# Performance work log

Measured on AMD Instinct MI355X. Metric: run time of the kernel, lower is better.

## Reference

```python
import jax, jax.numpy as jnp
import numpy as np

N, E, D, ED, L, B = 100000, 1600000, 128, 16, 5, 64
EPS = 1e-5


def _layer_norm(x, w, b):
    mu = jnp.mean(x, axis=-1, keepdims=True)
    var = jnp.mean((x - mu) ** 2, axis=-1, keepdims=True)
    return (x - mu) * jax.lax.rsqrt(var + EPS) * w + b


def setup_inputs() -> dict:
    key = jax.random.key(0)
    ks = jax.random.split(key, 10)
    sc = 0.05
    s = jax.random.normal(ks[0], (N, D), jnp.float32)
    edge_index = jax.random.randint(ks[1], (2, E), 0, N, dtype=jnp.int64)
    edge_attr = jax.random.normal(ks[2], (E, ED), jnp.float32)
    batch = jnp.sort(jax.random.randint(ks[3], (N,), 0, B, dtype=jnp.int64))
    return dict(
        s=s, edge_index=edge_index, edge_attr=edge_attr, batch=batch,
        ln_w=jnp.ones((L, D), jnp.float32),
        ln_b=jnp.zeros((L, D), jnp.float32),
        eW1=jax.random.normal(ks[4], (L, 2 * D + ED, ED), jnp.float32) * sc,
        eb1=jnp.zeros((L, ED), jnp.float32),
        eW2=jax.random.normal(ks[5], (L, ED, ED), jnp.float32) * sc,
        eb2=jnp.zeros((L, ED), jnp.float32),
        nW1=jax.random.normal(ks[6], (L, D + ED, D), jnp.float32) * sc,
        nb1=jnp.zeros((L, D), jnp.float32),
        nW2=jax.random.normal(ks[7], (L, D, D), jnp.float32) * sc,
        nb2=jnp.zeros((L, D), jnp.float32),
    )


def reference(s, edge_index, edge_attr, batch, ln_w, ln_b, eW1, eb1, eW2, eb2, nW1, nb1, nW2, nb2):
    src, dst = edge_index[0], edge_index[1]
    n = s.shape[0]
    num_layers = ln_w.shape[0]
    # scatter-mean denominator (in-degree, clamped to 1)
    deg = jax.ops.segment_sum(jnp.ones((edge_index.shape[1],), s.dtype), dst, num_segments=n)
    deg = jnp.maximum(deg, 1.0)[:, None]
    for i in range(num_layers):
        # per-node LayerNorm over feature dim (vector channel is None)
        s = _layer_norm(s, ln_w[i], ln_b[i])
        # edge message: gather endpoints, concat with edge_attr -> [E, 2D+ED]
        m = jnp.concatenate([s[src], s[dst], edge_attr], axis=-1)
        edge_attr = jax.nn.silu(m @ eW1[i] + eb1[i]) @ eW2[i] + eb2[i]
        # scatter-mean aggregate to destination nodes -> [N, ED]
        agg = jax.ops.segment_sum(edge_attr, dst, num_segments=n) / deg
        h = jnp.concatenate([s, agg], axis=-1)
        out = jax.nn.silu(h @ nW1[i] + nb1[i]) @ nW2[i] + nb2[i]  # discarded, as in original
    return s, edge_attr
```

## Files before the change

kernel.cpp:

```cpp
#include <hip/hip_runtime.h>

#define N_NODES 100000
#define N_EDGES 1600000
#define DIM     128
#define EDIM    16
#define NLAYERS 5

typedef unsigned short ushort_t;
typedef short bf16x8 __attribute__((ext_vector_type(8)));
typedef float f32x4  __attribute__((ext_vector_type(4)));

__device__ __forceinline__ ushort_t f2bf(float f) {
    union { float f; unsigned int i; } c; c.f = f;
    unsigned int r = c.i + 0x7fffu + ((c.i >> 16) & 1u);
    return (ushort_t)(r >> 16);
}
__device__ __forceinline__ float lo_bf(unsigned int w) {
    union { unsigned int i; float f; } c; c.i = w << 16; return c.f;
}
__device__ __forceinline__ float hi_bf(unsigned int w) {
    union { unsigned int i; float f; } c; c.i = w & 0xffff0000u; return c.f;
}
__device__ __forceinline__ unsigned int pk_bf16(float lo, float hi) {
    unsigned int r;
    asm("v_cvt_pk_bf16_f32 %0, %1, %2" : "=v"(r) : "v"(lo), "v"(hi));
    return r;
}
__device__ __forceinline__ bf16x8 pk8(f32x4 a, f32x4 b) {
    union { unsigned int w[4]; bf16x8 v; } c;
    c.w[0] = pk_bf16(a[0], a[1]); c.w[1] = pk_bf16(a[2], a[3]);
    c.w[2] = pk_bf16(b[0], b[1]); c.w[3] = pk_bf16(b[2], b[3]);
    return c.v;
}
__device__ __forceinline__ float fast_silu(float x) {
    return x * __builtin_amdgcn_rcpf(1.0f + __expf(-x));
}
__device__ __forceinline__ void lds_fence() {
    asm volatile("s_waitcnt lgkmcnt(0)" ::: "memory");
    __builtin_amdgcn_sched_barrier(0);
}

__global__ void swizzle_weights(const float* __restrict__ eW1,
                                const float* __restrict__ eW2,
                                const float* __restrict__ eb1,
                                const float* __restrict__ eb2,
                                ushort_t* __restrict__ w1s,
                                ushort_t* __restrict__ w2s,
                                ushort_t* __restrict__ wcs,
                                float* __restrict__ bcs) {
    int id = blockIdx.x * 256 + threadIdx.x;
    const int base = NLAYERS * 10 * 64;
    if (id < base) {
        int lane = id & 63;
        int t10 = id >> 6;
        int layer = t10 / 10, t = t10 % 10;
        int n = lane & 15, quad = lane >> 4;
        if (t < 9) {
            ushort_t* dst = w1s + ((size_t)(layer * 9 + t) * 64 + lane) * 8;
            #pragma unroll
            for (int j = 0; j < 8; ++j) {
                int k = t * 32 + quad * 8 + j;
                dst[j] = (k < 2 * DIM + EDIM)
                           ? f2bf(eW1[((size_t)layer * 272 + k) * 16 + n])
                           : (ushort_t)0;
            }
        } else {
            ushort_t* dst = w2s + ((size_t)layer * 64 + lane) * 8;
            #pragma unroll
            for (int j = 0; j < 8; ++j) {
                int k = quad * 8 + j;
                dst[j] = (k < EDIM) ? f2bf(eW2[((size_t)layer * 16 + k) * 16 + n])
                                    : (ushort_t)0;
            }
        }
    } else if (id < base + 4 * 64) {
        int id2 = id - base;
        int l = id2 >> 6;
        int lane = id2 & 63, n = lane & 15, quad = lane >> 4;
        ushort_t* dst = wcs + ((size_t)l * 64 + lane) * 8;
        #pragma unroll
        for (int j = 0; j < 8; ++j) {
            int r = quad * 8 + j;
            float acc = 0.f;
            if (r < EDIM)
                for (int k = 0; k < EDIM; ++k)
                    acc += eW2[((size_t)l * 16 + r) * 16 + k]
                         * eW1[((size_t)(l + 1) * 272 + 256 + k) * 16 + n];
            dst[j] = (r < EDIM) ? f2bf(acc) : (ushort_t)0;
        }
    } else if (id < base + 4 * 64 + 64) {
        int id2 = id - base - 4 * 64;
        int l = id2 >> 4, n = id2 & 15;
        float acc = eb1[(l + 1) * 16 + n];
        for (int k = 0; k < EDIM; ++k)
            acc += eb2[l * 16 + k] * eW1[((size_t)(l + 1) * 272 + 256 + k) * 16 + n];
        bcs[l * 16 + n] = acc;
    }
}

__global__ __launch_bounds__(256) void ln_uv(
        const float* __restrict__ sin, float* __restrict__ sout,
        const float* __restrict__ lnw, const float* __restrict__ lnb,
        const ushort_t* __restrict__ w1s,
        ushort_t* __restrict__ u_buf, ushort_t* __restrict__ v_buf,
        int l0, int l1, int lstr) {
    const int wv = threadIdx.x >> 6, lane = threadIdx.x & 63;
    const int m = lane & 15, quad = lane >> 4;
    const int tile = blockIdx.x * 4 + wv;
    if (tile >= N_NODES / 16) return;
    const int node = tile * 16 + m;

    float x[32];
    {
        const float* row = sin + (size_t)node * DIM + quad * 8;
        #pragma unroll
        for (int t = 0; t < 4; ++t) {
            f32x4 a = *(const f32x4*)(row + t * 32);
            f32x4 b = *(const f32x4*)(row + t * 32 + 4);
            #pragma unroll
            for (int j = 0; j < 4; ++j) { x[t * 8 + j] = a[j]; x[t * 8 + 4 + j] = b[j]; }
        }
    }

    for (int li = l0; li < l1; ++li) {
        float s = 0.f;
        #pragma unroll
        for (int k = 0; k < 32; ++k) s += x[k];
        s += __shfl_xor(s, 16); s += __shfl_xor(s, 32);
        float mu = s * (1.0f / DIM);
        float ss = 0.f;
        #pragma unroll
        for (int k = 0; k < 32; ++k) { float d = x[k] - mu; ss += d * d; }
        ss += __shfl_xor(ss, 16); ss += __shfl_xor(ss, 32);
        float rs = rsqrtf(ss * (1.0f / DIM) + 1e-5f);

        const float* w = lnw + (size_t)li * DIM + quad * 8;
        const float* b = lnb + (size_t)li * DIM + quad * 8;
        f32x4 au = {0.f, 0.f, 0.f, 0.f}, av = {0.f, 0.f, 0.f, 0.f};
        #pragma unroll
        for (int t = 0; t < 4; ++t) {
            f32x4 wa = *(const f32x4*)(w + t * 32), wb = *(const f32x4*)(w + t * 32 + 4);
            f32x4 ba = *(const f32x4*)(b + t * 32), bb = *(const f32x4*)(b + t * 32 + 4);
            #pragma unroll
            for (int j = 0; j < 4; ++j) {
                x[t * 8 + j]     = (x[t * 8 + j]     - mu) * rs * wa[j] + ba[j];
                x[t * 8 + 4 + j] = (x[t * 8 + 4 + j] - mu) * rs * wb[j] + bb[j];
            }
            f32x4 ya, yb;
            #pragma unroll
            for (int j = 0; j < 4; ++j) { ya[j] = x[t * 8 + j]; yb[j] = x[t * 8 + 4 + j]; }
            bf16x8 af = pk8(ya, yb);
            bf16x8 bu = *(const bf16x8*)(w1s + ((size_t)(li * 9 + t)     * 64 + lane) * 8);
            bf16x8 bv = *(const bf16x8*)(w1s + ((size_t)(li * 9 + 4 + t) * 64 + lane) * 8);
            au = __builtin_amdgcn_mfma_f32_16x16x32_bf16(bu, af, au, 0, 0, 0);
            av = __builtin_amdgcn_mfma_f32_16x16x32_bf16(bv, af, av, 0, 0, 0);
        }
        size_t rec = ((size_t)node * lstr + (li - l0)) * EDIM + quad * 4;
        uint2 tu; tu.x = pk_bf16(au[0], au[1]); tu.y = pk_bf16(au[2], au[3]);
        uint2 tv; tv.x = pk_bf16(av[0], av[1]); tv.y = pk_bf16(av[2], av[3]);
        *(uint2*)(u_buf + rec) = tu;
        *(uint2*)(v_buf + rec) = tv;
    }

    float* orow = sout + (size_t)node * DIM + quad * 8;
    #pragma unroll
    for (int t = 0; t < 4; ++t) {
        f32x4 a, b;
        #pragma unroll
        for (int j = 0; j < 4; ++j) { a[j] = x[t * 8 + j]; b[j] = x[t * 8 + 4 + j]; }
        *(f32x4*)(orow + t * 32) = a;
        *(f32x4*)(orow + t * 32 + 4) = b;
    }
}

template<int NL>
__global__ __launch_bounds__(256) void edge_fused(
        const float* __restrict__ ea_in, float* __restrict__ ea_out,
        const int* __restrict__ ei,
        const ushort_t* __restrict__ u_buf, const ushort_t* __restrict__ v_buf,
        const ushort_t* __restrict__ w1s, const ushort_t* __restrict__ w2s,
        const ushort_t* __restrict__ wcs, const float* __restrict__ bcs,
        const float* __restrict__ eb1, const float* __restrict__ eb2,
        int l0) {
    __shared__ ushort_t tbH[4][16 * 24];
    const int wv = threadIdx.x >> 6, lane = threadIdx.x & 63;
    const int m = lane & 15, quad = lane >> 4;

    const bf16x8 w1f0 = *(const bf16x8*)(w1s + (((size_t)l0 * 9 + 8) * 64 + lane) * 8);
    const bf16x8 w2f  = *(const bf16x8*)(w2s + ((size_t)(l0 + NL - 1) * 64 + lane) * 8);
    bf16x8 wcf[NL > 1 ? NL - 1 : 1];
    #pragma unroll
    for (int l = 1; l < NL; ++l)
        wcf[l - 1] = *(const bf16x8*)(wcs + ((size_t)(l0 + l - 1) * 64 + lane) * 8);
    f32x4 bx[NL], b2v;
    #pragma unroll
    for (int r = 0; r < 4; ++r) {
        bx[0][r] = eb1[l0 * EDIM + quad * 4 + r];
        b2v[r]   = eb2[(l0 + NL - 1) * EDIM + quad * 4 + r];
    }
    #pragma unroll
    for (int l = 1; l < NL; ++l)
        #pragma unroll
        for (int r = 0; r < 4; ++r)
            bx[l][r] = bcs[(l0 + l - 1) * EDIM + quad * 4 + r];

    ushort_t* tlH = tbH[wv];
    const bf16x8 zf = {0, 0, 0, 0, 0, 0, 0, 0};
    const f32x4 z4 = {0.f, 0.f, 0.f, 0.f};
    const int nTiles = N_EDGES / 64;
    const int stride = gridDim.x;

    int tile = blockIdx.x;
    if (tile >= nTiles) return;

    uint2 gu[NL], gv[NL];
    f32x4 ea_a = z4, ea_b = z4;
    int es_n, ed_n;
    {
        const int e0 = tile * 64 + wv * 16 + m;
        const int es = ei[e0];
        const int ed = ei[N_EDGES + e0];
        #pragma unroll
        for (int l = 0; l < NL; ++l) {
            gu[l] = *(const uint2*)(u_buf + ((size_t)es * NL + l) * EDIM + quad * 4);
            gv[l] = *(const uint2*)(v_buf + ((size_t)ed * NL + l) * EDIM + quad * 4);
        }
        if (quad < 2) {
            const float* ep = ea_in + (size_t)e0 * EDIM + quad * 8;
            ea_a = *(const f32x4*)ep; ea_b = *(const f32x4*)(ep + 4);
        }
        const int t1 = tile + stride;
        const int e1 = (t1 < nTiles ? t1 : tile) * 64 + wv * 16 + m;
        es_n = ei[e1];
        ed_n = ei[N_EDGES + e1];
    }

    for (; tile < nTiles; tile += stride) {
        const int tn = tile + stride;
        const bool hn = tn < nTiles;
        const int tc = hn ? tn : tile;

        uint2 gun[NL], gvn[NL];
        #pragma unroll
        for (int l = 0; l < NL; ++l) {
            gun[l] = *(const uint2*)(u_buf + ((size_t)es_n * NL + l) * EDIM + quad * 4);
            gvn[l] = *(const uint2*)(v_buf + ((size_t)ed_n * NL + l) * EDIM + quad * 4);
        }
        f32x4 ean_a = z4, ean_b = z4;
        {
            const int en = tc * 64 + wv * 16 + m;
            if (quad < 2) {
                const float* ep = ea_in + (size_t)en * EDIM + quad * 8;
                ean_a = *(const f32x4*)ep; ean_b = *(const f32x4*)(ep + 4);
            }
        }
        int es_nn, ed_nn;
        {
            const int t2 = tn + stride;
            const int e2 = (t2 < nTiles ? t2 : tc) * 64 + wv * 16 + m;
            es_nn = ei[e2];
            ed_nn = ei[N_EDGES + e2];
        }

        f32x4 hv;
        {
            bf16x8 af = zf;
            if (quad < 2) af = pk8(ea_a, ea_b);
            f32x4 acc = __builtin_amdgcn_mfma_f32_16x16x32_bf16(w1f0, af, z4, 0, 0, 0);
            hv[0] = fast_silu(acc[0] + lo_bf(gu[0].x) + lo_bf(gv[0].x) + bx[0][0]);
            hv[1] = fast_silu(acc[1] + hi_bf(gu[0].x) + hi_bf(gv[0].x) + bx[0][1]);
            hv[2] = fast_silu(acc[2] + lo_bf(gu[0].y) + lo_bf(gv[0].y) + bx[0][2]);
            hv[3] = fast_silu(acc[3] + hi_bf(gu[0].y) + hi_bf(gv[0].y) + bx[0][3]);
        }
        #pragma unroll
        for (int l = 1; l < NL; ++l) {
            uint2 hw; hw.x = pk_bf16(hv[0], hv[1]); hw.y = pk_bf16(hv[2], hv[3]);
            *(uint2*)(tlH + m * 24 + quad * 4) = hw;
            lds_fence();
            bf16x8 hf = zf;
            if (quad < 2) hf = *(const bf16x8*)(tlH + m * 24 + quad * 8);

            f32x4 acc = __builtin_amdgcn_mfma_f32_16x16x32_bf16(wcf[l - 1], hf, z4, 0, 0, 0);
            hv[0] = fast_silu(acc[0] + lo_bf(gu[l].x) + lo_bf(gv[l].x) + bx[l][0]);
            hv[1] = fast_silu(acc[1] + hi_bf(gu[l].x) + hi_bf(gv[l].x) + bx[l][1]);
            hv[2] = fast_silu(acc[2] + lo_bf(gu[l].y) + lo_bf(gv[l].y) + bx[l][2]);
            hv[3] = fast_silu(acc[3] + hi_bf(gu[l].y) + hi_bf(gv[l].y) + bx[l][3]);
        }
        f32x4 y;
        {
            uint2 hw; hw.x = pk_bf16(hv[0], hv[1]); hw.y = pk_bf16(hv[2], hv[3]);
            *(uint2*)(tlH + m * 24 + quad * 4) = hw;
            lds_fence();
            bf16x8 hf = zf;
            if (quad < 2) hf = *(const bf16x8*)(tlH + m * 24 + quad * 8);
            f32x4 acc2 = __builtin_amdgcn_mfma_f32_16x16x32_bf16(w2f, hf, z4, 0, 0, 0);
            y[0] = acc2[0] + b2v[0];
            y[1] = acc2[1] + b2v[1];
            y[2] = acc2[2] + b2v[2];
            y[3] = acc2[3] + b2v[3];
        }
        const int e = tile * 64 + wv * 16 + m;
        *(f32x4*)(ea_out + (size_t)e * EDIM + quad * 4) = y;

        #pragma unroll
        for (int l = 0; l < NL; ++l) { gu[l] = gun[l]; gv[l] = gvn[l]; }
        ea_a = ean_a; ea_b = ean_b;
        es_n = es_nn; ed_n = ed_nn;
    }
}

extern "C" void kernel_launch(void* const* d_in, const int* in_sizes, int n_in,
                              void* d_out, int out_size, void* d_ws, size_t ws_size,
                              hipStream_t stream) {
    const float* s_in  = (const float*)d_in[0];
    const int*   ei    = (const int*)d_in[1];
    const float* ea_in = (const float*)d_in[2];
    const float* lnw = (const float*)d_in[4];
    const float* lnb = (const float*)d_in[5];
    const float* eW1 = (const float*)d_in[6];
    const float* eb1 = (const float*)d_in[7];
    const float* eW2 = (const float*)d_in[8];
    const float* eb2 = (const float*)d_in[9];

    float* out_s  = (float*)d_out;
    float* out_ea = (float*)d_out + (size_t)N_NODES * DIM;

    ushort_t* w1s = (ushort_t*)d_ws;
    ushort_t* w2s = w1s + (size_t)NLAYERS * 9 * 64 * 8;
    ushort_t* wcs = w2s + (size_t)NLAYERS * 64 * 8;
    float*    bcs = (float*)(wcs + 4 * 64 * 8);
    ushort_t* uv0 = wcs + 4 * 64 * 8 + 128;
    const size_t wWords  = (size_t)NLAYERS * 10 * 64 * 8 + 4 * 64 * 8 + 128;
    const size_t uvLayer = (size_t)N_NODES * EDIM;
    const size_t needFused = (wWords + 2 * (size_t)NLAYERS * uvLayer) * 2;
    const int lnGrid = (N_NODES / 16 + 3) / 4;
    const int eGrid = 4096;

    swizzle_weights<<<14, 256, 0, stream>>>(eW1, eW2, eb1, eb2, w1s, w2s, wcs, bcs);

    if (ws_size >= needFused) {
        ushort_t* u0 = uv0;
        ushort_t* v0 = u0 + (size_t)NLAYERS * uvLayer;
        ln_uv<<<lnGrid, 256, 0, stream>>>(s_in, out_s, lnw, lnb, w1s,
                                          u0, v0, 0, NLAYERS, NLAYERS);
        edge_fused<NLAYERS><<<eGrid, 256, 0, stream>>>(ea_in, out_ea, ei, u0, v0,
                                                       w1s, w2s, wcs, bcs,
                                                       eb1, eb2, 0);
    } else {
        ushort_t* u0 = uv0;
        ushort_t* v0 = u0 + uvLayer;
        for (int l = 0; l < NLAYERS; ++l) {
            ln_uv<<<lnGrid, 256, 0, stream>>>(l == 0 ? s_in : out_s, out_s,
                                              lnw, lnb, w1s, u0, v0, l, l + 1, 1);
            edge_fused<1><<<eGrid, 256, 0, stream>>>(
                l == 0 ? ea_in : (const float*)out_ea, out_ea, ei, u0, v0,
                w1s, w2s, wcs, bcs, eb1, eb2, l);
        }
    }
}
```

Baseline: 431.3 us.

## Deepen edge-tile software pipeline to three in-flight gather stages

The edge-MLP loop moves from double buffering (gathers for the next tile) to a three-slot rotating buffer. Gathered u/v rows and edge attributes are kept three tiles ahead, and edge indices six tiles ahead. The aim is to hide more latency from the random gathers. The cost is many more live VGPRs, which can reduce occupancy, plus extra redundant loads through the clamped tile indices near the end.

```diff
diff --git a/kernel.cpp b/kernel.cpp
--- a/kernel.cpp
+++ b/kernel.cpp
@@ -209,104 +209,94 @@
     const f32x4 z4 = {0.f, 0.f, 0.f, 0.f};
     const int nTiles = N_EDGES / 64;
     const int stride = gridDim.x;
-
-    int tile = blockIdx.x;
-    if (tile >= nTiles) return;
-
-    uint2 gu[NL], gv[NL];
-    f32x4 ea_a = z4, ea_b = z4;
-    int es_n, ed_n;
-    {
-        const int e0 = tile * 64 + wv * 16 + m;
-        const int es = ei[e0];
-        const int ed = ei[N_EDGES + e0];
-        #pragma unroll
-        for (int l = 0; l < NL; ++l) {
-            gu[l] = *(const uint2*)(u_buf + ((size_t)es * NL + l) * EDIM + quad * 4);
-            gv[l] = *(const uint2*)(v_buf + ((size_t)ed * NL + l) * EDIM + quad * 4);
-        }
-        if (quad < 2) {
-            const float* ep = ea_in + (size_t)e0 * EDIM + quad * 8;
-            ea_a = *(const f32x4*)ep; ea_b = *(const f32x4*)(ep + 4);
-        }
-        const int t1 = tile + stride;
-        const int e1 = (t1 < nTiles ? t1 : tile) * 64 + wv * 16 + m;
-        es_n = ei[e1];
-        ed_n = ei[N_EDGES + e1];
-    }
-
-    for (; tile < nTiles; tile += stride) {
-        const int tn = tile + stride;
-        const bool hn = tn < nTiles;
-        const int tc = hn ? tn : tile;
-
-        uint2 gun[NL], gvn[NL];
-        #pragma unroll
-        for (int l = 0; l < NL; ++l) {
-            gun[l] = *(const uint2*)(u_buf + ((size_t)es_n * NL + l) * EDIM + quad * 4);
-            gvn[l] = *(const uint2*)(v_buf + ((size_t)ed_n * NL + l) * EDIM + quad * 4);
-        }
-        f32x4 ean_a = z4, ean_b = z4;
-        {
-            const int en = tc * 64 + wv * 16 + m;
-            if (quad < 2) {
-                const float* ep = ea_in + (size_t)en * EDIM + quad * 8;
-                ean_a = *(const f32x4*)ep; ean_b = *(const f32x4*)(ep + 4);
-            }
-        }
-        int es_nn, ed_nn;
-        {
-            const int t2 = tn + stride;
-            const int e2 = (t2 < nTiles ? t2 : tc) * 64 + wv * 16 + m;
-            es_nn = ei[e2];
-            ed_nn = ei[N_EDGES + e2];
-        }
-
-        f32x4 hv;
-        {
-            bf16x8 af = zf;
-            if (quad < 2) af = pk8(ea_a, ea_b);
-            f32x4 acc = __builtin_amdgcn_mfma_f32_16x16x32_bf16(w1f0, af, z4, 0, 0, 0);
-            hv[0] = fast_silu(acc[0] + lo_bf(gu[0].x) + lo_bf(gv[0].x) + bx[0][0]);
-            hv[1] = fast_silu(acc[1] + hi_bf(gu[0].x) + hi_bf(gv[0].x) + bx[0][1]);
-            hv[2] = fast_silu(acc[2] + lo_bf(gu[0].y) + lo_bf(gv[0].y) + bx[0][2]);
-            hv[3] = fast_silu(acc[3] + hi_bf(gu[0].y) + hi_bf(gv[0].y) + bx[0][3]);
-        }
-        #pragma unroll
-        for (int l = 1; l < NL; ++l) {
-            uint2 hw; hw.x = pk_bf16(hv[0], hv[1]); hw.y = pk_bf16(hv[2], hv[3]);
-            *(uint2*)(tlH + m * 24 + quad * 4) = hw;
-            lds_fence();
-            bf16x8 hf = zf;
-            if (quad < 2) hf = *(const bf16x8*)(tlH + m * 24 + quad * 8);
-
-            f32x4 acc = __builtin_amdgcn_mfma_f32_16x16x32_bf16(wcf[l - 1], hf, z4, 0, 0, 0);
-            hv[0] = fast_silu(acc[0] + lo_bf(gu[l].x) + lo_bf(gv[l].x) + bx[l][0]);
-            hv[1] = fast_silu(acc[1] + hi_bf(gu[l].x) + hi_bf(gv[l].x) + bx[l][1]);
-            hv[2] = fast_silu(acc[2] + lo_bf(gu[l].y) + lo_bf(gv[l].y) + bx[l][2]);
-            hv[3] = fast_silu(acc[3] + hi_bf(gu[l].y) + hi_bf(gv[l].y) + bx[l][3]);
-        }
-        f32x4 y;
-        {
-            uint2 hw; hw.x = pk_bf16(hv[0], hv[1]); hw.y = pk_bf16(hv[2], hv[3]);
-            *(uint2*)(tlH + m * 24 + quad * 4) = hw;
-            lds_fence();
-            bf16x8 hf = zf;
-            if (quad < 2) hf = *(const bf16x8*)(tlH + m * 24 + quad * 8);
-            f32x4 acc2 = __builtin_amdgcn_mfma_f32_16x16x32_bf16(w2f, hf, z4, 0, 0, 0);
-            y[0] = acc2[0] + b2v[0];
-            y[1] = acc2[1] + b2v[1];
-            y[2] = acc2[2] + b2v[2];
-            y[3] = acc2[3] + b2v[3];
-        }
-        const int e = tile * 64 + wv * 16 + m;
-        *(f32x4*)(ea_out + (size_t)e * EDIM + quad * 4) = y;
-
-        #pragma unroll
-        for (int l = 0; l < NL; ++l) { gu[l] = gun[l]; gv[l] = gvn[l]; }
-        ea_a = ean_a; ea_b = ean_b;
-        es_n = es_nn; ed_n = ed_nn;
-    }
+    const int t0 = blockIdx.x;
+    if (t0 >= nTiles) return;
+    const int eoff = wv * 16 + m;
+
+    uint2 guA[NL], gvA[NL]; f32x4 eaAa, eaAb;
+    uint2 guB[NL], gvB[NL]; f32x4 eaBa, eaBb;
+    uint2 guC[NL], gvC[NL]; f32x4 eaCa, eaCb;
+    int esA, edA, esB, edB, esC, edC;
+
+#define CLAMPT(t) ((t) < nTiles ? (t) : t0)
+#define LOAD_EI(S, t) do { int _e = (t) * 64 + eoff;                         \
+        es##S = ei[_e]; ed##S = ei[N_EDGES + _e]; } while (0)
+#define LOAD_GA(S) do { _Pragma("unroll")                                    \
+    for (int _l = 0; _l < NL; ++_l) {                                        \
+        gu##S[_l] = *(const uint2*)(u_buf + ((size_t)es##S * NL + _l) * EDIM + quad * 4); \
+        gv##S[_l] = *(const uint2*)(v_buf + ((size_t)ed##S * NL + _l) * EDIM + quad * 4); \
+    } } while (0)
+#define LOAD_EA(S, t) do { ea##S##a = z4; ea##S##b = z4; if (quad < 2) {     \
+        const float* _p = ea_in + (size_t)((t) * 64 + eoff) * EDIM + quad * 8; \
+        ea##S##a = *(const f32x4*)_p; ea##S##b = *(const f32x4*)(_p + 4); } } while (0)
+#define COMPUTE_STORE(S, tv) do {                                            \
+    f32x4 hv;                                                                \
+    {   bf16x8 af = zf;                                                      \
+        if (quad < 2) af = pk8(ea##S##a, ea##S##b);                          \
+        f32x4 acc = __builtin_amdgcn_mfma_f32_16x16x32_bf16(w1f0, af, z4, 0, 0, 0); \
+        hv[0] = fast_silu(acc[0] + lo_bf(gu##S[0].x) + lo_bf(gv##S[0].x) + bx[0][0]); \
+        hv[1] = fast_silu(acc[1] + hi_bf(gu##S[0].x) + hi_bf(gv##S[0].x) + bx[0][1]); \
+        hv[2] = fast_silu(acc[2] + lo_bf(gu##S[0].y) + lo_bf(gv##S[0].y) + bx[0][2]); \
+        hv[3] = fast_silu(acc[3] + hi_bf(gu##S[0].y) + hi_bf(gv##S[0].y) + bx[0][3]); \
+    }                                                                        \
+    _Pragma("unroll")                                                        \
+    for (int _l = 1; _l < NL; ++_l) {                                        \
+        uint2 hw; hw.x = pk_bf16(hv[0], hv[1]); hw.y = pk_bf16(hv[2], hv[3]); \
+        *(uint2*)(tlH + m * 24 + quad * 4) = hw;                             \
+        lds_fence();                                                         \
+        bf16x8 hf = zf;                                                      \
+        if (quad < 2) hf = *(const bf16x8*)(tlH + m * 24 + quad * 8);        \
+        f32x4 acc = __builtin_amdgcn_mfma_f32_16x16x32_bf16(wcf[_l - 1], hf, z4, 0, 0, 0); \
+        hv[0] = fast_silu(acc[0] + lo_bf(gu##S[_l].x) + lo_bf(gv##S[_l].x) + bx[_l][0]); \
+        hv[1] = fast_silu(acc[1] + hi_bf(gu##S[_l].x) + hi_bf(gv##S[_l].x) + bx[_l][1]); \
+        hv[2] = fast_silu(acc[2] + lo_bf(gu##S[_l].y) + lo_bf(gv##S[_l].y) + bx[_l][2]); \
+        hv[3] = fast_silu(acc[3] + hi_bf(gu##S[_l].y) + hi_bf(gv##S[_l].y) + bx[_l][3]); \
+    }                                                                        \
+    f32x4 y;                                                                 \
+    {   uint2 hw; hw.x = pk_bf16(hv[0], hv[1]); hw.y = pk_bf16(hv[2], hv[3]); \
+        *(uint2*)(tlH + m * 24 + quad * 4) = hw;                             \
+        lds_fence();                                                         \
+        bf16x8 hf = zf;                                                      \
+        if (quad < 2) hf = *(const bf16x8*)(tlH + m * 24 + quad * 8);        \
+        f32x4 acc2 = __builtin_amdgcn_mfma_f32_16x16x32_bf16(w2f, hf, z4, 0, 0, 0); \
+        y[0] = acc2[0] + b2v[0]; y[1] = acc2[1] + b2v[1];                    \
+        y[2] = acc2[2] + b2v[2]; y[3] = acc2[3] + b2v[3];                    \
+    }                                                                        \
+    *(f32x4*)(ea_out + (size_t)((tv) * 64 + eoff) * EDIM + quad * 4) = y;    \
+    } while (0)
+
+    LOAD_EI(A, t0);
+    LOAD_EI(B, CLAMPT(t0 + stride));
+    LOAD_EI(C, CLAMPT(t0 + 2 * stride));
+    LOAD_GA(A); LOAD_EA(A, t0);
+    LOAD_GA(B); LOAD_EA(B, CLAMPT(t0 + stride));
+    LOAD_GA(C); LOAD_EA(C, CLAMPT(t0 + 2 * stride));
+    LOAD_EI(A, CLAMPT(t0 + 3 * stride));
+    LOAD_EI(B, CLAMPT(t0 + 4 * stride));
+    LOAD_EI(C, CLAMPT(t0 + 5 * stride));
+
+    int tile = t0;
+    for (;;) {
+        COMPUTE_STORE(A, tile);
+        LOAD_GA(A); LOAD_EA(A, CLAMPT(tile + 3 * stride));
+        LOAD_EI(A, CLAMPT(tile + 6 * stride));
+        tile += stride; if (tile >= nTiles) break;
+
+        COMPUTE_STORE(B, tile);
+        LOAD_GA(B); LOAD_EA(B, CLAMPT(tile + 3 * stride));
+        LOAD_EI(B, CLAMPT(tile + 6 * stride));
+        tile += stride; if (tile >= nTiles) break;
+
+        COMPUTE_STORE(C, tile);
+        LOAD_GA(C); LOAD_EA(C, CLAMPT(tile + 3 * stride));
+        LOAD_EI(C, CLAMPT(tile + 6 * stride));
+        tile += stride; if (tile >= nTiles) break;
+    }
+#undef CLAMPT
+#undef LOAD_EI
+#undef LOAD_GA
+#undef LOAD_EA
+#undef COMPUTE_STORE
 }
 
 extern "C" void kernel_launch(void* const* d_in, const int* in_sizes, int n_in,
```

After: 461.7 us. 7.0% more time.
